# Performance work log

Hardware: AMD Instinct MI355X
Metric: run time of the kernel (lower is better)

## Reference

```python
import jax, jax.numpy as jnp
import numpy as np

B, T, E, H = 4, 2048, 1024, 16
D = E // H  # head_size = 64

def setup_inputs() -> dict:
    key = jax.random.key(0)
    ks = jax.random.split(key, 8)
    s = 1.0 / np.sqrt(E)
    inp = {
        'k': jax.random.normal(ks[0], (B, T, E), jnp.float32),
        'q': jax.random.normal(ks[1], (B, T, E), jnp.float32),
        'v': jax.random.normal(ks[2], (B, T, E), jnp.float32),
        'mask': jnp.triu(jnp.ones((T, T), jnp.bool_), k=1),  # True above diagonal -> masked
        # per-head projection weights stacked: [H, E, D], no bias (bias=False)
        'Wk': jax.random.uniform(ks[3], (H, E, D), jnp.float32, -s, s),
        'Wq': jax.random.uniform(ks[4], (H, E, D), jnp.float32, -s, s),
        'Wv': jax.random.uniform(ks[5], (H, E, D), jnp.float32, -s, s),
        # output projection (bias=True default)
        'Wp': jax.random.uniform(ks[6], (E, E), jnp.float32, -s, s),
        'bp': jax.random.uniform(ks[7], (E,), jnp.float32, -s, s),
    }
    return inp

def reference(k, q, v, mask, Wk, Wq, Wv, Wp, bp):
    # per-head projections (bias=False Linears), batched over heads
    xk = jnp.einsum('bte,hed->bhtd', k, Wk)
    xq = jnp.einsum('bte,hed->bhtd', q, Wq)
    xv = jnp.einsum('bte,hed->bhtd', v, Wv)
    # NOTE: original scales by sqrt(C) where C = embed_size (input dim), not head_size
    wei = jnp.einsum('bhtd,bhsd->bhts', xq, xk) / jnp.sqrt(jnp.asarray(E, xq.dtype))
    wei = jnp.where(mask, -jnp.inf, wei)  # masked_fill(mask, -inf)
    wei = jax.nn.softmax(wei, axis=-1)
    out = jnp.einsum('bhts,bhsd->bhtd', wei, xv)
    out = out.transpose(0, 2, 1, 3).reshape(B, T, E)  # concat heads on last dim
    return out @ Wp.T + bp
```

## Files before the change

### kernel.cpp

```cpp
#include <hip/hip_runtime.h>
#include <cstdint>
#include <cstddef>


#define B_ 4
#define T_ 2048
#define E_ 1024
#define H_ 16
#define D_ 64
#define MROWS 8192
#define MK    8388608
#define SCALE_LOG2E 0.045084220027780106f

typedef unsigned short u16;
typedef unsigned int   u32;
typedef __attribute__((ext_vector_type(4))) float  f32x4;
typedef __attribute__((ext_vector_type(4))) u32    u32x4;
typedef __attribute__((ext_vector_type(8))) u16    u16x8;
typedef __attribute__((ext_vector_type(8))) __bf16 bf16x8;

typedef __attribute__((address_space(1))) void gvoid_t;
typedef __attribute__((address_space(3))) void lvoid_t;

__device__ __forceinline__ void async_load16(const void* g, void* l) {
  __builtin_amdgcn_global_load_lds((gvoid_t*)(uintptr_t)g, (lvoid_t*)l, 16, 0, 0);
}

__device__ __forceinline__ u16 f2bf(float f) {
  u32 u = __builtin_bit_cast(u32, f);
  u = (u + 0x7FFFu + ((u >> 16) & 1u)) >> 16;
  return (u16)u;
}

__device__ __forceinline__ bf16x8 ldfrag(const u16* p) {
  u32x4 t = *(const u32x4*)p;
  return __builtin_bit_cast(bf16x8, t);
}

__device__ __forceinline__ bf16x8 ldfrag_g(const u16* p) {
  u32x4 t = *(const u32x4*)p;
  return __builtin_bit_cast(bf16x8, t);
}

__device__ __forceinline__ f32x4 mfma_bf16(bf16x8 a, bf16x8 b, f32x4 c) {
  return __builtin_amdgcn_mfma_f32_16x16x32_bf16(a, b, c, 0, 0, 0);
}

__global__ __launch_bounds__(256) void cast_qkv_kernel(
    const float* __restrict__ q, const float* __restrict__ k,
    const float* __restrict__ v, u16* __restrict__ dst) {
  const int z = blockIdx.y;
  const float* src = (z == 0) ? q : (z == 1) ? k : v;
  const float sc = (z == 0) ? SCALE_LOG2E : 1.0f;
  u16* out = dst + (size_t)z * MK;
  size_t i0 = ((size_t)blockIdx.x * 256 + threadIdx.x) * 8;
  float4 a = *(const float4*)(src + i0);
  float4 b = *(const float4*)(src + i0 + 4);
  u16x8 o;
  o[0] = f2bf(a.x * sc); o[1] = f2bf(a.y * sc);
  o[2] = f2bf(a.z * sc); o[3] = f2bf(a.w * sc);
  o[4] = f2bf(b.x * sc); o[5] = f2bf(b.y * sc);
  o[6] = f2bf(b.z * sc); o[7] = f2bf(b.w * sc);
  *(u16x8*)(out + i0) = o;
}

__global__ __launch_bounds__(256) void prep_weights_kernel(
    const float* __restrict__ Wq, const float* __restrict__ Wk,
    const float* __restrict__ Wv, const float* __restrict__ Wp,
    u16* __restrict__ dstW, u16* __restrict__ dstWp) {
  const int z = blockIdx.y;
  const int t = blockIdx.x * 256 + threadIdx.x;
  if (z == 3) { dstWp[t] = f2bf(Wp[t]); return; }
  const float* W = (z == 0) ? Wq : (z == 1) ? Wk : Wv;
  const int j = t >> 10, e = t & 1023;
  const int h = j >> 6, d = j & 63;
  dstW[(size_t)z * (E_ * E_) + t] = f2bf(W[h * (E_ * D_) + e * D_ + d]);
}

template <int FINAL>
__global__ __launch_bounds__(256) void gemm_bt_kernel(
    const u16* __restrict__ Abase, const u16* __restrict__ Btbase,
    u16* __restrict__ Cb, float* __restrict__ Cf,
    const float* __restrict__ bias) {
  constexpr int Md = 8192, Nd = 1024, Kd = 1024;
  __shared__ __align__(16) u16 As[128 * 32];
  __shared__ __align__(16) u16 Bs[128 * 32];
  const int tid = threadIdx.x;
  const int wave = tid >> 6, lane = tid & 63;
  const int l16 = lane & 15, quad = lane >> 4;
  const int z = blockIdx.z;
  const u16* A  = Abase  + (size_t)z * Md * Kd;
  const u16* Bt = Btbase + (size_t)z * Nd * Kd;
  const int tm = blockIdx.x * 128, tn = blockIdx.y * 128;
  const int wm = (wave >> 1) * 64, wn = (wave & 1) * 64;

  f32x4 acc[4][4];
#pragma unroll
  for (int i = 0; i < 4; ++i)
#pragma unroll
    for (int j = 0; j < 4; ++j) acc[i][j] = f32x4{0.f, 0.f, 0.f, 0.f};

  const int row0 = tid >> 2, seg = tid & 3;
  const u16* Ag0 = A  + (size_t)(tm + row0) * Kd + seg * 8;
  const u16* Ag1 = Ag0 + (size_t)64 * Kd;
  const u16* Bg0 = Bt + (size_t)(tn + row0) * Kd + seg * 8;
  const u16* Bg1 = Bg0 + (size_t)64 * Kd;
  char* AsB = (char*)&As[0];
  char* BsB = (char*)&Bs[0];
  const int wbase = wave * 1024;

  for (int kt = 0; kt < Kd / 32; ++kt) {
    async_load16(Ag0, AsB + wbase);
    async_load16(Ag1, AsB + 4096 + wbase);
    async_load16(Bg0, BsB + wbase);
    async_load16(Bg1, BsB + 4096 + wbase);
    Ag0 += 32; Ag1 += 32; Bg0 += 32; Bg1 += 32;
    __syncthreads();
    bf16x8 af[4], bfr[4];
#pragma unroll
    for (int i = 0; i < 4; ++i) {
      af[i]  = ldfrag(&As[(wm + i * 16 + l16) * 32 + quad * 8]);
      bfr[i] = ldfrag(&Bs[(wn + i * 16 + l16) * 32 + quad * 8]);
    }
#pragma unroll
    for (int mi = 0; mi < 4; ++mi)
#pragma unroll
      for (int ni = 0; ni < 4; ++ni)
        acc[mi][ni] = mfma_bf16(af[mi], bfr[ni], acc[mi][ni]);
    __syncthreads();
  }

  if (FINAL) {
    float bv[4];
#pragma unroll
    for (int ni = 0; ni < 4; ++ni) bv[ni] = bias[tn + wn + ni * 16 + l16];
#pragma unroll
    for (int mi = 0; mi < 4; ++mi)
#pragma unroll
      for (int r = 0; r < 4; ++r) {
        const int row = tm + wm + mi * 16 + quad * 4 + r;
        float* cp = Cf + (size_t)row * Nd + tn + wn;
#pragma unroll
        for (int ni = 0; ni < 4; ++ni)
          cp[ni * 16 + l16] = acc[mi][ni][r] + bv[ni];
      }
  } else {
    u16* C = Cb + (size_t)z * Md * Nd;
#pragma unroll
    for (int mi = 0; mi < 4; ++mi)
#pragma unroll
      for (int r = 0; r < 4; ++r) {
        const int row = tm + wm + mi * 16 + quad * 4 + r;
        u16* cp = C + (size_t)row * Nd + tn + wn;
#pragma unroll
        for (int ni = 0; ni < 4; ++ni)
          cp[ni * 16 + l16] = f2bf(acc[mi][ni][r]);
      }
  }
}

__global__ __launch_bounds__(256, 4) void attn_kernel(
    const u16* __restrict__ Xq, const u16* __restrict__ Xk,
    const u16* __restrict__ Xv, u16* __restrict__ Xo) {
  const int qt = 15 - blockIdx.y;
  const int bh = blockIdx.x;
  const int b = bh >> 4, h = bh & 15;
  const int tid = threadIdx.x, wave = tid >> 6, lane = tid & 63;
  const int l16 = lane & 15, quad = lane >> 4;

  __shared__ __align__(16) u16 Ks[2 * 64 * 32];
  __shared__ __align__(16) u16 Vts[64 * 72];
  __shared__ __align__(16) u16 Ps[128 * 72];

  const size_t base = (size_t)b * T_ * E_ + h * 64;
  const u16* Qp = Xq + base + (size_t)qt * 128 * E_;
  const u16* Kp = Xk + base;
  const u16* Vp = Xv + base;

  bf16x8 qf[2][2];
#pragma unroll
  for (int mi = 0; mi < 2; ++mi)
#pragma unroll
    for (int ks = 0; ks < 2; ++ks)
      qf[mi][ks] = ldfrag_g(Qp + (size_t)(wave * 32 + mi * 16 + l16) * E_ +
                            ks * 32 + quad * 8);

  u16x8 ones_u;
#pragma unroll
  for (int i = 0; i < 8; ++i) ones_u[i] = 0x3F80;
  const bf16x8 ones = __builtin_bit_cast(bf16x8, ones_u);

  f32x4 o_acc[2][4];
#pragma unroll
  for (int mi = 0; mi < 2; ++mi)
#pragma unroll
    for (int di = 0; di < 4; ++di) o_acc[mi][di] = f32x4{0.f, 0.f, 0.f, 0.f};
  f32x4 lrow[2] = {f32x4{0.f, 0.f, 0.f, 0.f}, f32x4{0.f, 0.f, 0.f, 0.f}};

  char* KsB = (char*)&Ks[0];
  const int kt_end = 2 * qt + 1;
  for (int kt = 0; kt <= kt_end; ++kt) {
#pragma unroll
    for (int i = 0; i < 2; ++i) {
      const int call = wave + i * 4;
      const int ks = call >> 2, rb = (call & 3) * 16;
      const int row = rb + (lane >> 2), k8 = lane & 3;
      async_load16(Kp + (size_t)(kt * 64 + row) * E_ + ks * 32 + k8 * 8,
                   KsB + ks * 4096 + rb * 64);
    }
#pragma unroll
    for (int i = 0; i < 2; ++i) {
      const int dseg = wave + i * 4;
      union { u32x4 v; u16 s[8]; } t;
      t.v = *(const u32x4*)(Vp + (size_t)(kt * 64 + lane) * E_ + dseg * 8);
#pragma unroll
      for (int ii = 0; ii < 8; ++ii)
        Vts[(dseg * 8 + ii) * 72 + lane] = t.s[ii];
    }
    __syncthreads();

    bf16x8 kf[4][2];
#pragma unroll
    for (int ni = 0; ni < 4; ++ni)
#pragma unroll
      for (int ks = 0; ks < 2; ++ks)
        kf[ni][ks] = ldfrag(&Ks[ks * 2048 + (ni * 16 + l16) * 32 + quad * 8]);

    f32x4 sa[2][4];
#pragma unroll
    for (int mi = 0; mi < 2; ++mi)
#pragma unroll
      for (int ni = 0; ni < 4; ++ni) {
        f32x4 s = f32x4{0.f, 0.f, 0.f, 0.f};
        s = mfma_bf16(qf[mi][0], kf[ni][0], s);
        s = mfma_bf16(qf[mi][1], kf[ni][1], s);
        sa[mi][ni] = s;
      }

    if (kt >= 2 * qt) {
#pragma unroll
      for (int mi = 0; mi < 2; ++mi) {
        const int grow0 = qt * 128 + wave * 32 + mi * 16 + quad * 4;
#pragma unroll
        for (int ni = 0; ni < 4; ++ni) {
          const int gcol = kt * 64 + ni * 16 + l16;
#pragma unroll
          for (int r = 0; r < 4; ++r)
            if (gcol > grow0 + r) sa[mi][ni][r] = -INFINITY;
        }
      }
    }

#pragma unroll
    for (int mi = 0; mi < 2; ++mi) {
#pragma unroll
      for (int ni = 0; ni < 4; ++ni)
#pragma unroll
        for (int r = 0; r < 4; ++r)
          sa[mi][ni][r] = exp2f(sa[mi][ni][r]);
#pragma unroll
      for (int ni = 0; ni < 4; ++ni)
#pragma unroll
        for (int r = 0; r < 4; ++r)
          Ps[(wave * 32 + mi * 16 + quad * 4 + r) * 72 + ni * 16 + l16] =
              f2bf(sa[mi][ni][r]);
    }

    bf16x8 pf[2][2], vf[4][2];
#pragma unroll
    for (int mi = 0; mi < 2; ++mi)
#pragma unroll
      for (int ks = 0; ks < 2; ++ks)
        pf[mi][ks] = ldfrag(&Ps[(wave * 32 + mi * 16 + l16) * 72 + ks * 32 + quad * 8]);
#pragma unroll
    for (int di = 0; di < 4; ++di)
#pragma unroll
      for (int ks = 0; ks < 2; ++ks)
        vf[di][ks] = ldfrag(&Vts[(di * 16 + l16) * 72 + ks * 32 + quad * 8]);
#pragma unroll
    for (int mi = 0; mi < 2; ++mi) {
      lrow[mi] = mfma_bf16(pf[mi][0], ones, lrow[mi]);
      lrow[mi] = mfma_bf16(pf[mi][1], ones, lrow[mi]);
#pragma unroll
      for (int di = 0; di < 4; ++di) {
        o_acc[mi][di] = mfma_bf16(pf[mi][0], vf[di][0], o_acc[mi][di]);
        o_acc[mi][di] = mfma_bf16(pf[mi][1], vf[di][1], o_acc[mi][di]);
      }
    }
    __syncthreads();
  }

  u16* Op = Xo + base + (size_t)qt * 128 * E_;
#pragma unroll
  for (int mi = 0; mi < 2; ++mi)
#pragma unroll
    for (int r = 0; r < 4; ++r) {
      const float inv = 1.0f / lrow[mi][r];
      const int row = wave * 32 + mi * 16 + quad * 4 + r;
#pragma unroll
      for (int di = 0; di < 4; ++di)
        Op[(size_t)row * E_ + di * 16 + l16] = f2bf(o_acc[mi][di][r] * inv);
    }
}

extern "C" void kernel_launch(void* const* d_in, const int* in_sizes, int n_in,
                              void* d_out, int out_size, void* d_ws, size_t ws_size,
                              hipStream_t stream) {
  const float* k_in = (const float*)d_in[0];
  const float* q_in = (const float*)d_in[1];
  const float* v_in = (const float*)d_in[2];
  const float* Wk = (const float*)d_in[4];
  const float* Wq = (const float*)d_in[5];
  const float* Wv = (const float*)d_in[6];
  const float* Wp = (const float*)d_in[7];
  const float* bp = (const float*)d_in[8];
  float* out = (float*)d_out;

  char* ws = (char*)d_ws;
  u16* qkvb = (u16*)ws;
  u16* Wt   = (u16*)(ws + 50331648);
  u16* Wpb  = (u16*)(ws + 56623104);
  u16* X    = (u16*)(ws + 58720256);
  u16* Xo   = (u16*)ws;

  cast_qkv_kernel<<<dim3(4096, 3), 256, 0, stream>>>(q_in, k_in, v_in, qkvb);
  prep_weights_kernel<<<dim3(4096, 4), 256, 0, stream>>>(Wq, Wk, Wv, Wp, Wt, Wpb);
  gemm_bt_kernel<0><<<dim3(64, 8, 3), 256, 0, stream>>>(qkvb, Wt, X, nullptr, nullptr);
  attn_kernel<<<dim3(64, 16), 256, 0, stream>>>(X, X + (size_t)MK, X + (size_t)2 * MK, Xo);
  gemm_bt_kernel<1><<<dim3(64, 8, 1), 256, 0, stream>>>(Xo, Wpb, nullptr, out, bp);
}
```

Measured before the change: 339.4 us.

## Double-buffer K/V tiles in attention loop to overlap loads with compute

K and V tiles in shared memory are now double-buffered. The next tile's async K load and V global load are issued while the current tile's QK^T, masking and exp run, and the transposed V is written into the other buffer before the PV MFMAs. This hides global memory latency behind compute and drops the trailing barrier, leaving one __syncthreads per iteration. In exchange the shared-memory footprint grows, and launch bounds drop from 4 to 3 blocks per CU, which lowers occupancy.

```diff
diff --git a/kernel.cpp b/kernel.cpp
--- a/kernel.cpp
+++ b/kernel.cpp
@@ -159,7 +159,7 @@
   }
 }
 
-__global__ __launch_bounds__(256, 4) void attn_kernel(
+__global__ __launch_bounds__(256, 3) void attn_kernel(
     const u16* __restrict__ Xq, const u16* __restrict__ Xk,
     const u16* __restrict__ Xv, u16* __restrict__ Xo) {
   const int qt = 15 - blockIdx.y;
@@ -168,14 +168,46 @@
   const int tid = threadIdx.x, wave = tid >> 6, lane = tid & 63;
   const int l16 = lane & 15, quad = lane >> 4;
 
-  __shared__ __align__(16) u16 Ks[2 * 64 * 32];
-  __shared__ __align__(16) u16 Vts[64 * 72];
+  __shared__ __align__(16) u16 Ks[2 * 4096];
+  __shared__ __align__(16) u16 Vts[2 * 4608];
   __shared__ __align__(16) u16 Ps[128 * 72];
 
   const size_t base = (size_t)b * T_ * E_ + h * 64;
   const u16* Qp = Xq + base + (size_t)qt * 128 * E_;
   const u16* Kp = Xk + base;
   const u16* Vp = Xv + base;
+  char* KsB = (char*)&Ks[0];
+
+  const int krow = ((wave & 3) * 16) + (lane >> 2);
+  const int kk8 = lane & 3;
+
+  auto stageK = [&](int kt, int buf) {
+#pragma unroll
+    for (int i = 0; i < 2; ++i) {
+      const int c = wave + i * 4;
+      const int ks = c >> 2, rb = (c & 3) * 16;
+      const int row = rb + (lane >> 2);
+      async_load16(Kp + (size_t)(kt * 64 + row) * E_ + ks * 32 + kk8 * 8,
+                   KsB + buf * 8192 + ks * 4096 + rb * 64);
+    }
+  };
+  auto loadV = [&](int kt, u32x4* vreg) {
+#pragma unroll
+    for (int i = 0; i < 2; ++i) {
+      const int dseg = wave + i * 4;
+      vreg[i] = *(const u32x4*)(Vp + (size_t)(kt * 64 + lane) * E_ + dseg * 8);
+    }
+  };
+  auto writeV = [&](int buf, const u32x4* vreg) {
+#pragma unroll
+    for (int i = 0; i < 2; ++i) {
+      const int dseg = wave + i * 4;
+      union { u32x4 v; u16 s[8]; } t; t.v = vreg[i];
+#pragma unroll
+      for (int ii = 0; ii < 8; ++ii)
+        Vts[buf * 4608 + (dseg * 8 + ii) * 72 + lane] = t.s[ii];
+    }
+  };
 
   bf16x8 qf[2][2];
 #pragma unroll
@@ -197,26 +229,16 @@
     for (int di = 0; di < 4; ++di) o_acc[mi][di] = f32x4{0.f, 0.f, 0.f, 0.f};
   f32x4 lrow[2] = {f32x4{0.f, 0.f, 0.f, 0.f}, f32x4{0.f, 0.f, 0.f, 0.f}};
 
-  char* KsB = (char*)&Ks[0];
+  {
+    u32x4 vreg[2];
+    stageK(0, 0);
+    loadV(0, vreg);
+    writeV(0, vreg);
+  }
+
   const int kt_end = 2 * qt + 1;
   for (int kt = 0; kt <= kt_end; ++kt) {
-#pragma unroll
-    for (int i = 0; i < 2; ++i) {
-      const int call = wave + i * 4;
-      const int ks = call >> 2, rb = (call & 3) * 16;
-      const int row = rb + (lane >> 2), k8 = lane & 3;
-      async_load16(Kp + (size_t)(kt * 64 + row) * E_ + ks * 32 + k8 * 8,
-                   KsB + ks * 4096 + rb * 64);
-    }
-#pragma unroll
-    for (int i = 0; i < 2; ++i) {
-      const int dseg = wave + i * 4;
-      union { u32x4 v; u16 s[8]; } t;
-      t.v = *(const u32x4*)(Vp + (size_t)(kt * 64 + lane) * E_ + dseg * 8);
-#pragma unroll
-      for (int ii = 0; ii < 8; ++ii)
-        Vts[(dseg * 8 + ii) * 72 + lane] = t.s[ii];
-    }
+    const int buf = kt & 1;
     __syncthreads();
 
     bf16x8 kf[4][2];
@@ -224,7 +246,8 @@
     for (int ni = 0; ni < 4; ++ni)
 #pragma unroll
       for (int ks = 0; ks < 2; ++ks)
-        kf[ni][ks] = ldfrag(&Ks[ks * 2048 + (ni * 16 + l16) * 32 + quad * 8]);
+        kf[ni][ks] = ldfrag(&Ks[buf * 4096 + ks * 2048 + (ni * 16 + l16) * 32 +
+                                quad * 8]);
 
     f32x4 sa[2][4];
 #pragma unroll
@@ -237,6 +260,13 @@
         sa[mi][ni] = s;
       }
 
+    u32x4 vreg[2];
+    const bool have_next = (kt < kt_end);
+    if (have_next) {
+      stageK(kt + 1, buf ^ 1);
+      loadV(kt + 1, vreg);
+    }
+
     if (kt >= 2 * qt) {
 #pragma unroll
       for (int mi = 0; mi < 2; ++mi) {
@@ -266,17 +296,21 @@
               f2bf(sa[mi][ni][r]);
     }
 
+    if (have_next) writeV(buf ^ 1, vreg);
+
     bf16x8 pf[2][2], vf[4][2];
 #pragma unroll
     for (int mi = 0; mi < 2; ++mi)
 #pragma unroll
       for (int ks = 0; ks < 2; ++ks)
-        pf[mi][ks] = ldfrag(&Ps[(wave * 32 + mi * 16 + l16) * 72 + ks * 32 + quad * 8]);
+        pf[mi][ks] = ldfrag(&Ps[(wave * 32 + mi * 16 + l16) * 72 + ks * 32 +
+                                quad * 8]);
 #pragma unroll
     for (int di = 0; di < 4; ++di)
 #pragma unroll
       for (int ks = 0; ks < 2; ++ks)
-        vf[di][ks] = ldfrag(&Vts[(di * 16 + l16) * 72 + ks * 32 + quad * 8]);
+        vf[di][ks] = ldfrag(&Vts[buf * 4608 + (di * 16 + l16) * 72 + ks * 32 +
+                                 quad * 8]);
 #pragma unroll
     for (int mi = 0; mi < 2; ++mi) {
       lrow[mi] = mfma_bf16(pf[mi][0], ones, lrow[mi]);
@@ -287,7 +321,6 @@
         o_acc[mi][di] = mfma_bf16(pf[mi][1], vf[di][1], o_acc[mi][di]);
       }
     }
-    __syncthreads();
   }
 
   u16* Op = Xo + base + (size_t)qt * 128 * E_;
```

After: 331.3 us. 1.02x faster.
